# Optimization experiments

Hardware: AMD Instinct MI355X
Metric: run time of the kernel (lower is better)

Reference implementation:

```python
import jax, jax.numpy as jnp
import numpy as np

B, C, L, O = 32, 256, 336, 96
K, NLAYERS, DFF = 4, 2, 1024
EPS = 1e-5


def setup_inputs() -> dict:
    key = jax.random.key(0)
    ks = jax.random.split(key, 10)
    s1 = 1.0 / np.sqrt(L)
    s2 = 1.0 / np.sqrt(DFF)
    return {
        "x": jax.random.normal(ks[0], (B, C, L), dtype=jnp.float32),
        "rev_w": jnp.ones((C,), dtype=jnp.float32),
        "rev_b": jnp.zeros((C,), dtype=jnp.float32),
        "W1": jax.random.normal(ks[1], (K, NLAYERS, L, DFF), dtype=jnp.float32) * s1,
        "b1": jnp.zeros((K, NLAYERS, DFF), dtype=jnp.float32),
        "W2": jax.random.normal(ks[2], (K, NLAYERS, DFF, L), dtype=jnp.float32) * s2,
        "b2": jnp.zeros((K, NLAYERS, L), dtype=jnp.float32),
        "Wh": jax.random.normal(ks[3], (K, L, O), dtype=jnp.float32) * s1,
        "bh": jnp.zeros((K, O), dtype=jnp.float32),
        "assign": jax.random.randint(ks[4], (C,), 0, K, dtype=jnp.int32),
    }


def reference(x, rev_w, rev_b, W1, b1, W2, b2, Wh, bh, assign):
    # RevIN norm over the time axis, per instance and per channel. x: [B,C,L]
    mean = jnp.mean(x, axis=-1, keepdims=True)
    std = jnp.sqrt(jnp.var(x, axis=-1, keepdims=True) + EPS)
    xn = (x - mean) / std * rev_w[None, :, None] + rev_b[None, :, None]

    n_clusters = Wh.shape[0]
    n_layers = W1.shape[1]
    out = jnp.zeros(x.shape[:2] + (Wh.shape[-1],), dtype=x.dtype)  # [B,C,O]
    for k in range(n_clusters):
        z = xn  # [B,C,L] time-mixing MLP stack shared across channels
        for l in range(n_layers):
            h = jax.nn.relu(jnp.einsum('bcl,ld->bcd', z, W1[k, l]) + b1[k, l])
            z = z + jnp.einsum('bcd,dl->bcl', h, W2[k, l]) + b2[k, l]
        y = jnp.einsum('bcl,lo->bco', z, Wh[k]) + bh[k]  # [B,C,O]
        out = jnp.where((assign == k)[None, :, None], y, out)

    # RevIN denorm, then transpose to [B, out_len, C]
    out = (out - rev_b[None, :, None]) / rev_w[None, :, None] * std + mean
    return jnp.transpose(out, (0, 2, 1))
```

## Files before the change

kernel.cpp:

```cpp
#include <hip/hip_runtime.h>
#include <math.h>


typedef unsigned short u16;
typedef unsigned int u32;
typedef unsigned long long u64;

constexpr int B = 32, C = 256, L = 336, O = 96, K = 4, NL = 2, DFF = 1024;
constexpr int TM = 32;
constexpr int NTILES = (B * C) / TM;
constexpr int LP = 352;
constexpr int ZBS = 360;
constexpr int HS = 1032;

constexpr int DT1 = 32;
constexpr int KT1 = 22;
constexpr int LT2 = 11;
constexpr int KT2 = 64;
constexpr int NTH = 6;
constexpr int KSH = 11;

constexpr int TS1 = KT1 * 512;
constexpr int TS2 = KT2 * 512;
constexpr int THS = KSH * 512;

constexpr int W1FRAGS = DT1 * KT1 * 64;
constexpr int W2FRAGS = LT2 * KT2 * 64;
constexpr int WHFRAGS = NTH * KSH * 64;
constexpr int NW1 = W1FRAGS * K * NL;
constexpr int NW2 = W2FRAGS * K * NL;
constexpr int NPREP = 176 + 256 + 44 + 1;

typedef __bf16 bf16x8 __attribute__((ext_vector_type(8)));
typedef float f32x4 __attribute__((ext_vector_type(4)));
typedef float f32x16 __attribute__((ext_vector_type(16)));

__device__ float g_y[(size_t)B * O * C];

__device__ __forceinline__ u16 f2bf(float f) {
  union { float f; u32 u; } v;
  v.f = f;
  u32 r = v.u + 0x7fffu + ((v.u >> 16) & 1u);
  return (u16)(r >> 16);
}
__device__ __forceinline__ float bf2f(u16 h) {
  union { u32 u; float f; } v;
  v.u = ((u32)h) << 16;
  return v.f;
}
__device__ __forceinline__ u32 pack2(float a, float b) {
  return (u32)f2bf(a) | ((u32)f2bf(b) << 16);
}

__global__ __launch_bounds__(256) void prep(const int* __restrict__ assign,
                                            const float* __restrict__ W1,
                                            const float* __restrict__ W2,
                                            const float* __restrict__ Wh,
                                            int* __restrict__ meta,
                                            u16* __restrict__ wbuf) {
  __shared__ u16 sm[32][516];
  const int bid = blockIdx.x;
  const int tid = threadIdx.x;
  const int wid = tid >> 6, lane = tid & 63;
  const int q = lane >> 4, rm = lane & 15;
  const int q2 = lane >> 5, n32 = lane & 31;

  if (bid < 176) {
    const int dh = bid & 1;
    const int ks32 = (bid >> 1) % 11;
    const int kl = bid / 22;
    for (int rr = 0; rr < 8; ++rr) {
      const int r = wid * 8 + rr;
      const int l = ks32 * 32 + r;
#pragma unroll
      for (int h = 0; h < 2; ++h) {
        const int c = h * 256 + lane * 4;
        float4 v = make_float4(0.f, 0.f, 0.f, 0.f);
        if (l < L)
          v = *(const float4*)(W1 + ((size_t)kl * L + l) * DFF + dh * 512 + c);
        uint2 p;
        p.x = pack2(v.x, v.y);
        p.y = pack2(v.z, v.w);
        *(uint2*)&sm[r][c] = p;
      }
    }
    __syncthreads();
    for (int e = 0; e < 8; ++e) {
      const int item = wid * 8 + e;
      const int dtl = item >> 1, half = item & 1;
      const int rb = 16 * half + q2 * 8;
      const int col = dtl * 32 + n32;
      uint4 o;
      u32 w4[4];
#pragma unroll
      for (int jj = 0; jj < 4; ++jj)
        w4[jj] = (u32)sm[rb + 2 * jj][col] | ((u32)sm[rb + 2 * jj + 1][col] << 16);
      o.x = w4[0]; o.y = w4[1]; o.z = w4[2]; o.w = w4[3];
      const int dt = dh * 16 + dtl;
      const int ks = ks32 * 2 + half;
      *(uint4*)(wbuf + ((size_t)(kl * DT1 + dt) * KT1 + ks) * 512 + lane * 8) = o;
    }
  } else if (bid < 432) {
    const int b2i = bid - 176;
    const int ks32 = b2i & 31;
    const int kl = b2i >> 5;
    for (int rr = 0; rr < 8; ++rr) {
      const int r = wid * 8 + rr;
      const float* row = W2 + ((size_t)kl * DFF + ks32 * 32 + r) * L;
      {
        const int c = lane * 4;
        const float4 v = *(const float4*)(row + c);
        uint2 p;
        p.x = pack2(v.x, v.y);
        p.y = pack2(v.z, v.w);
        *(uint2*)&sm[r][c] = p;
      }
      {
        const int c = 256 + lane * 4;
        if (c < 352) {
          float4 v = make_float4(0.f, 0.f, 0.f, 0.f);
          if (c < L) v = *(const float4*)(row + c);
          uint2 p;
          p.x = pack2(v.x, v.y);
          p.y = pack2(v.z, v.w);
          *(uint2*)&sm[r][c] = p;
        }
      }
    }
    __syncthreads();
    for (int item = wid; item < 22; item += 4) {
      const int lt = item >> 1, half = item & 1;
      const int rb = 16 * half + q2 * 8;
      const int col = 32 * lt + n32;
      uint4 o;
      u32 w4[4];
#pragma unroll
      for (int jj = 0; jj < 4; ++jj)
        w4[jj] = (u32)sm[rb + 2 * jj][col] | ((u32)sm[rb + 2 * jj + 1][col] << 16);
      o.x = w4[0]; o.y = w4[1]; o.z = w4[2]; o.w = w4[3];
      const int ks = ks32 * 2 + half;
      *(uint4*)(wbuf + (size_t)NW1 * 8 +
                ((size_t)(kl * LT2 + lt) * KT2 + ks) * 512 + lane * 8) = o;
    }
  } else if (bid < 476) {
    const int b3i = bid - 432;
    const int ks = b3i % 11;
    const int kk = b3i / 11;
    for (int rr = 0; rr < 8; ++rr) {
      const int r = wid * 8 + rr;
      const int l = ks * 32 + r;
      if (lane < 24) {
        const int c = lane * 4;
        float4 v = make_float4(0.f, 0.f, 0.f, 0.f);
        if (l < L) v = *(const float4*)(Wh + ((size_t)kk * L + l) * O + c);
        uint2 p;
        p.x = pack2(v.x, v.y);
        p.y = pack2(v.z, v.w);
        *(uint2*)&sm[r][c] = p;
      }
    }
    __syncthreads();
    for (int nt = wid; nt < NTH; nt += 4) {
      uint4 o;
      u32 w4[4];
#pragma unroll
      for (int jj = 0; jj < 4; ++jj) {
        const u16 a = sm[q * 8 + 2 * jj][nt * 16 + rm];
        const u16 b = sm[q * 8 + 2 * jj + 1][nt * 16 + rm];
        w4[jj] = (u32)a | ((u32)b << 16);
      }
      o.x = w4[0]; o.y = w4[1]; o.z = w4[2]; o.w = w4[3];
      *(uint4*)(wbuf + (size_t)(NW1 + NW2) * 8 +
                ((size_t)(kk * NTH + nt) * KSH + ks) * 512 + lane * 8) = o;
    }
  } else {
    __shared__ int wcnt[4][K];
    __shared__ int pre[4][K];
    __shared__ int cofs[K + 1];
    const int a = assign[tid];
    const u64 below = (1ull << lane) - 1ull;
    int myrank = 0;
#pragma unroll
    for (int k = 0; k < K; ++k) {
      const u64 m = __ballot(a == k);
      if (a == k) myrank = (int)__popcll(m & below);
      if (lane == 0) wcnt[wid][k] = (int)__popcll(m);
    }
    __syncthreads();
    if (tid == 0) {
      int tot[K];
      for (int k = 0; k < K; ++k) {
        int s = 0;
        for (int ww = 0; ww < 4; ++ww) {
          pre[ww][k] = s;
          s += wcnt[ww][k];
        }
        tot[k] = s;
      }
      cofs[0] = 0;
      for (int k = 0; k < K; ++k) cofs[k + 1] = cofs[k] + tot[k];
      for (int k = 0; k <= K; ++k) meta[512 + k] = cofs[k];
    }
    __syncthreads();
    const int pos = cofs[a] + pre[wid][a] + myrank;
    meta[256 + pos] = tid;
    meta[520 + tid] = pos;
    int k = 0;
    while (k < K - 1 && tid >= cofs[k + 1]) ++k;
    meta[tid] = (k << 16) | ((tid - cofs[k]) * TM);
  }
}

__global__ __launch_bounds__(1024, 4) void mlp_mfma(
    const float* __restrict__ x, const float* __restrict__ rev_w,
    const float* __restrict__ rev_b, const float* __restrict__ b1,
    const float* __restrict__ b2, const float* __restrict__ bh,
    const int* __restrict__ meta, const u16* __restrict__ wbuf) {
  __shared__ __align__(16) u16 zb[TM][ZBS];
  __shared__ __align__(16) u16 Hsh[TM][HS];
  __shared__ float s_mean[TM], s_std[TM], s_rw[TM], s_rb[TM];
  __shared__ int s_b[TM], s_p[TM];

  const int tid = threadIdx.x;
  const int wid = tid >> 6;
  const int lane = tid & 63;
  const int q = lane >> 4, rm = lane & 15;
  const int q2 = lane >> 5, n32 = lane & 31;

  const int swz = (blockIdx.x & 7) * 32 + (blockIdx.x >> 3);
  const int info = meta[swz];
  const int kcl = info >> 16;
  const int rstart = info & 0xffff;
  const int cofs = meta[512 + kcl];
  const int cnt = meta[512 + kcl + 1] - cofs;

  for (int i = 0; i < 2; ++i) {
    const int t = wid * 2 + i;
    const int ri = rstart + t;
    const int b = ri / cnt;
    const int c = meta[256 + cofs + (ri % cnt)];
    const float* xrow = x + (size_t)(b * C + c) * L;
    float v[6], s = 0.f, s2 = 0.f;
#pragma unroll
    for (int jj = 0; jj < 6; ++jj) {
      const int j = lane + jj * 64;
      v[jj] = (j < L) ? xrow[j] : 0.f;
      s += v[jj];
      s2 += v[jj] * v[jj];
    }
#pragma unroll
    for (int off = 32; off > 0; off >>= 1) {
      s += __shfl_down(s, off);
      s2 += __shfl_down(s2, off);
    }
    s = __shfl(s, 0);
    s2 = __shfl(s2, 0);
    const float mean = s * (1.f / L);
    const float var = s2 * (1.f / L) - mean * mean;
    const float stdv = sqrtf(var + 1e-5f);
    const float rstd = 1.f / stdv;
    const float rw = rev_w[c], rb_ = rev_b[c];
#pragma unroll
    for (int jj = 0; jj < 6; ++jj) {
      const int j = lane + jj * 64;
      if (j < L) zb[t][j] = f2bf((v[jj] - mean) * rstd * rw + rb_);
    }
    if (lane < LP - L) zb[t][L + lane] = 0;
    if (lane == 0) {
      s_mean[t] = mean;
      s_std[t] = stdv;
      s_rw[t] = rw;
      s_rb[t] = rb_;
      s_b[t] = b;
      s_p[t] = cofs + (ri % cnt);
    }
  }

  const u16* w1b = wbuf;
  const u16* w2b = wbuf + (size_t)NW1 * 8;
  const u16* whb = wbuf + (size_t)(NW1 + NW2) * 8;

  bf16x8 a1[2][4];
  {
    const u16* b0 = w1b + (size_t)(kcl * NL) * W1FRAGS * 8 +
                    (size_t)(wid * 2) * TS1 + lane * 8;
#pragma unroll
    for (int t = 0; t < 2; ++t)
#pragma unroll
      for (int s = 0; s < 4; ++s)
        a1[t][s] = *(const bf16x8*)(b0 + (size_t)t * TS1 + s * 512);
  }
  __syncthreads();

  f32x16 zm;
#pragma unroll
  for (int i = 0; i < 16; ++i) zm[i] = 0.f;
  if (wid < LT2) {
#pragma unroll
    for (int g = 0; g < 4; ++g) {
      const uint2 zw = *(const uint2*)&zb[n32][32 * wid + 8 * g + 4 * q2];
      zm[4 * g + 0] = bf2f((u16)zw.x);
      zm[4 * g + 1] = bf2f((u16)(zw.x >> 16));
      zm[4 * g + 2] = bf2f((u16)zw.y);
      zm[4 * g + 3] = bf2f((u16)(zw.y >> 16));
    }
  }

  for (int l = 0; l < NL; ++l) {
    const int kl = kcl * NL + l;
    const u16* W1f = w1b + (size_t)kl * W1FRAGS * 8;
    const u16* W2f = w2b + (size_t)kl * W2FRAGS * 8;
    const float* b1p = b1 + kl * DFF;
    const float* b2p = b2 + kl * L;
    const u16* base1 = W1f + (size_t)(wid * 2) * TS1 + lane * 8;

    f32x16 acc[2];
#pragma unroll
    for (int t = 0; t < 2; ++t)
#pragma unroll
      for (int i = 0; i < 16; ++i) acc[t][i] = 0.f;
#pragma unroll
    for (int ks = 0; ks < KT1; ++ks) {
      const bf16x8 zf = *(const bf16x8*)&zb[n32][ks * 16 + q2 * 8];
#pragma unroll
      for (int t = 0; t < 2; ++t)
        acc[t] = __builtin_amdgcn_mfma_f32_32x32x16_bf16(a1[t][ks & 3], zf,
                                                         acc[t], 0, 0, 0);
      if (ks + 4 < KT1) {
#pragma unroll
        for (int t = 0; t < 2; ++t)
          a1[t][ks & 3] =
              *(const bf16x8*)(base1 + (size_t)t * TS1 + (ks + 4) * 512);
      }
    }
#pragma unroll
    for (int t = 0; t < 2; ++t) {
      const int dt = wid * 2 + t;
#pragma unroll
      for (int g = 0; g < 4; ++g) {
        const int db = dt * 32 + 8 * g + 4 * q2;
        const float4 bq = *(const float4*)(b1p + db);
        uint2 hw;
        hw.x = pack2(fmaxf(acc[t][4 * g + 0] + bq.x, 0.f),
                     fmaxf(acc[t][4 * g + 1] + bq.y, 0.f));
        hw.y = pack2(fmaxf(acc[t][4 * g + 2] + bq.z, 0.f),
                     fmaxf(acc[t][4 * g + 3] + bq.w, 0.f));
        *(uint2*)&Hsh[n32][db] = hw;
      }
    }

    bf16x8 a2[8];
    const u16* base2 = W2f + (size_t)wid * TS2 + lane * 8;
    if (wid < LT2) {
#pragma unroll
      for (int s = 0; s < 8; ++s)
        a2[s] = *(const bf16x8*)(base2 + s * 512);
    }
    __syncthreads();

    if (wid < LT2) {
#pragma unroll
      for (int ks = 0; ks < KT2; ++ks) {
        const bf16x8 hf = *(const bf16x8*)&Hsh[n32][ks * 16 + q2 * 8];
        zm = __builtin_amdgcn_mfma_f32_32x32x16_bf16(a2[ks & 7], hf, zm, 0, 0, 0);
        if (ks + 8 < KT2)
          a2[ks & 7] = *(const bf16x8*)(base2 + (ks + 8) * 512);
      }
#pragma unroll
      for (int g = 0; g < 4; ++g) {
        const int lc = 32 * wid + 8 * g + 4 * q2;
        if (lc < L) {
          const float4 bq = *(const float4*)(b2p + lc);
          zm[4 * g + 0] += bq.x;
          zm[4 * g + 1] += bq.y;
          zm[4 * g + 2] += bq.z;
          zm[4 * g + 3] += bq.w;
        }
        uint2 zw;
        zw.x = pack2(zm[4 * g + 0], zm[4 * g + 1]);
        zw.y = pack2(zm[4 * g + 2], zm[4 * g + 3]);
        *(uint2*)&zb[n32][lc] = zw;
      }
    }

    if (l + 1 < NL) {
      const u16* nb = w1b + (size_t)(kl + 1) * W1FRAGS * 8 +
                      (size_t)(wid * 2) * TS1 + lane * 8;
#pragma unroll
      for (int t = 0; t < 2; ++t)
#pragma unroll
        for (int s = 0; s < 4; ++s)
          a1[t][s] = *(const bf16x8*)(nb + (size_t)t * TS1 + s * 512);
    }
    __syncthreads();
  }

  if (wid < NTH) {
    const u16* Whf =
        whb + (size_t)kcl * WHFRAGS * 8 + (size_t)wid * THS + lane * 8;
    f32x4 acc0 = {0.f, 0.f, 0.f, 0.f}, acc1 = {0.f, 0.f, 0.f, 0.f};
    for (int ks = 0; ks < KSH; ++ks) {
      const bf16x8 af = *(const bf16x8*)(Whf + ks * 512);
      const bf16x8 zf0 = *(const bf16x8*)&zb[rm][ks * 32 + q * 8];
      const bf16x8 zf1 = *(const bf16x8*)&zb[rm + 16][ks * 32 + q * 8];
      acc0 = __builtin_amdgcn_mfma_f32_16x16x32_bf16(af, zf0, acc0, 0, 0, 0);
      acc1 = __builtin_amdgcn_mfma_f32_16x16x32_bf16(af, zf1, acc1, 0, 0, 0);
    }
    const float4 bq = *(const float4*)(bh + kcl * O + wid * 16 + q * 4);
    const float bqa[4] = {bq.x, bq.y, bq.z, bq.w};
#pragma unroll
    for (int rg = 0; rg < 2; ++rg) {
      const int row = rm + 16 * rg;
      const float mean = s_mean[row], stdv = s_std[row];
      const float rw = s_rw[row], rb_ = s_rb[row];
      const int ob = s_b[row], pp = s_p[row];
      const f32x4 acc = rg ? acc1 : acc0;
#pragma unroll
      for (int gg = 0; gg < 4; ++gg) {
        const int o = wid * 16 + q * 4 + gg;
        const float v = acc[gg] + bqa[gg];
        g_y[((size_t)ob * O + o) * C + pp] = (v - rb_) / rw * stdv + mean;
      }
    }
  }
}

__global__ __launch_bounds__(1024) void scatter_out(
    const int* __restrict__ meta, float* __restrict__ out) {
  const int row = blockIdx.x * 4 + (threadIdx.x >> 8);
  const int c = threadIdx.x & 255;
  const int p = meta[520 + c];
  out[(size_t)row * C + c] = g_y[(size_t)row * C + p];
}

extern "C" void kernel_launch(void* const* d_in, const int* in_sizes, int n_in,
                              void* d_out, int out_size, void* d_ws,
                              size_t ws_size, hipStream_t stream) {
  const float* x = (const float*)d_in[0];
  const float* rev_w = (const float*)d_in[1];
  const float* rev_b = (const float*)d_in[2];
  const float* W1 = (const float*)d_in[3];
  const float* b1 = (const float*)d_in[4];
  const float* W2 = (const float*)d_in[5];
  const float* b2 = (const float*)d_in[6];
  const float* Wh = (const float*)d_in[7];
  const float* bh = (const float*)d_in[8];
  const int* assign = (const int*)d_in[9];
  float* out = (float*)d_out;

  int* meta = (int*)d_ws;
  u16* wbuf = (u16*)((char*)d_ws + 4096);

  prep<<<NPREP, 256, 0, stream>>>(assign, W1, W2, Wh, meta, wbuf);
  mlp_mfma<<<NTILES, 1024, 0, stream>>>(x, rev_w, rev_b, b1, b2, bh, meta,
                                        wbuf);
  scatter_out<<<(B * O) / 4, 1024, 0, stream>>>(meta, out);
}
```

Before: 145.8 us.

## Fuse prep, MLP and scatter into one cooperative kernel with grid syncs

Replaces the three-launch sequence (weight repack/meta prep, MLP, output scatter) with a single cooperative kernel of 256 blocks that uses grid-wide syncs between phases. The weight repack work is spread across all blocks in XCD-aware order, which removes two kernel launch gaps and their inter-kernel idle time. In exchange it adds two grid barriers and shares LDS between the repack and the MLP. If the cooperative launch fails it falls back to the old three-kernel path.

```diff
diff --git a/kernel.cpp b/kernel.cpp
--- a/kernel.cpp
+++ b/kernel.cpp
@@ -1,5 +1,8 @@
 #include <hip/hip_runtime.h>
+#include <hip/hip_cooperative_groups.h>
 #include <math.h>
+
+namespace cg = cooperative_groups;
 
 
 typedef unsigned short u16;
@@ -52,6 +55,409 @@
   return (u32)f2bf(a) | ((u32)f2bf(b) << 16);
 }
 
+__global__ __launch_bounds__(1024, 4) void mono(
+    const float* __restrict__ x, const float* __restrict__ rev_w,
+    const float* __restrict__ rev_b, const float* __restrict__ W1,
+    const float* __restrict__ b1, const float* __restrict__ W2,
+    const float* __restrict__ b2, const float* __restrict__ Wh,
+    const float* __restrict__ bh, const int* __restrict__ assign,
+    int* __restrict__ meta, u16* __restrict__ wbuf,
+    float* __restrict__ out) {
+  __shared__ __align__(16) u16 zb[TM][ZBS];
+  __shared__ __align__(16) u16 Hsh[TM][HS];
+  __shared__ float s_mean[TM], s_std[TM], s_rw[TM], s_rb[TM];
+  __shared__ int s_b[TM], s_p[TM];
+  __shared__ int t_wcnt[4][K], t_pre[4][K], t_cofs[K + 1];
+
+  const int bid = blockIdx.x;
+  const int tid = threadIdx.x;
+  const int wid = tid >> 6;
+  const int lane = tid & 63;
+  const int q = lane >> 4, rm = lane & 15;
+  const int q2 = lane >> 5, n32 = lane & 31;
+
+  u16(*sm)[516] = (u16(*)[516]) & Hsh[0][0];
+
+  {
+    const int xcd = bid & 7;
+    const int cser = xcd >> 1;
+    const int jj2 = ((xcd & 1) << 5) + (bid >> 3);
+    for (int t2 = 0; t2 < 2; ++t2) {
+      const int iu = jj2 * 2 + t2;
+      if (iu < 119) {
+        __syncthreads();
+        if (iu < 44) {
+          const int dh = iu & 1;
+          const int ks32 = (iu >> 1) % 11;
+          const int kl = cser * 2 + iu / 22;
+          for (int rr = 0; rr < 2; ++rr) {
+            const int r = wid * 2 + rr;
+            const int l = ks32 * 32 + r;
+#pragma unroll
+            for (int h = 0; h < 2; ++h) {
+              const int cc = h * 256 + lane * 4;
+              float4 v = make_float4(0.f, 0.f, 0.f, 0.f);
+              if (l < L)
+                v = *(const float4*)(W1 + ((size_t)kl * L + l) * DFF +
+                                     dh * 512 + cc);
+              uint2 p;
+              p.x = pack2(v.x, v.y);
+              p.y = pack2(v.z, v.w);
+              *(uint2*)&sm[r][cc] = p;
+            }
+          }
+          __syncthreads();
+          for (int e = 0; e < 2; ++e) {
+            const int item = wid * 2 + e;
+            const int dtl = item >> 1, half = item & 1;
+            const int rb = 16 * half + q2 * 8;
+            const int col = dtl * 32 + n32;
+            u32 w4[4];
+#pragma unroll
+            for (int t4 = 0; t4 < 4; ++t4)
+              w4[t4] = (u32)sm[rb + 2 * t4][col] |
+                       ((u32)sm[rb + 2 * t4 + 1][col] << 16);
+            uint4 o;
+            o.x = w4[0]; o.y = w4[1]; o.z = w4[2]; o.w = w4[3];
+            const int dt = dh * 16 + dtl;
+            const int ks = ks32 * 2 + half;
+            *(uint4*)(wbuf + ((size_t)(kl * DT1 + dt) * KT1 + ks) * 512 +
+                      lane * 8) = o;
+          }
+        } else if (iu < 108) {
+          const int i2 = iu - 44;
+          const int ks32 = i2 & 31;
+          const int kl = cser * 2 + (i2 >> 5);
+          for (int rr = 0; rr < 2; ++rr) {
+            const int r = wid * 2 + rr;
+            const float* row = W2 + ((size_t)kl * DFF + ks32 * 32 + r) * L;
+            {
+              const int cc = lane * 4;
+              const float4 v = *(const float4*)(row + cc);
+              uint2 p;
+              p.x = pack2(v.x, v.y);
+              p.y = pack2(v.z, v.w);
+              *(uint2*)&sm[r][cc] = p;
+            }
+            {
+              const int cc = 256 + lane * 4;
+              if (cc < 352) {
+                float4 v = make_float4(0.f, 0.f, 0.f, 0.f);
+                if (cc < L) v = *(const float4*)(row + cc);
+                uint2 p;
+                p.x = pack2(v.x, v.y);
+                p.y = pack2(v.z, v.w);
+                *(uint2*)&sm[r][cc] = p;
+              }
+            }
+          }
+          __syncthreads();
+          for (int item = wid; item < 22; item += 16) {
+            const int lt = item >> 1, half = item & 1;
+            const int rb = 16 * half + q2 * 8;
+            const int col = 32 * lt + n32;
+            u32 w4[4];
+#pragma unroll
+            for (int t4 = 0; t4 < 4; ++t4)
+              w4[t4] = (u32)sm[rb + 2 * t4][col] |
+                       ((u32)sm[rb + 2 * t4 + 1][col] << 16);
+            uint4 o;
+            o.x = w4[0]; o.y = w4[1]; o.z = w4[2]; o.w = w4[3];
+            const int ks = ks32 * 2 + half;
+            *(uint4*)(wbuf + (size_t)NW1 * 8 +
+                      ((size_t)(kl * LT2 + lt) * KT2 + ks) * 512 + lane * 8) =
+                o;
+          }
+        } else {
+          const int ks = iu - 108;
+          const int kk = cser;
+          for (int rr = 0; rr < 2; ++rr) {
+            const int r = wid * 2 + rr;
+            const int l = ks * 32 + r;
+            if (lane < 24) {
+              const int cc = lane * 4;
+              float4 v = make_float4(0.f, 0.f, 0.f, 0.f);
+              if (l < L)
+                v = *(const float4*)(Wh + ((size_t)kk * L + l) * O + cc);
+              uint2 p;
+              p.x = pack2(v.x, v.y);
+              p.y = pack2(v.z, v.w);
+              *(uint2*)&sm[r][cc] = p;
+            }
+          }
+          __syncthreads();
+          if (wid < NTH) {
+            const int nt = wid;
+            u32 w4[4];
+#pragma unroll
+            for (int t4 = 0; t4 < 4; ++t4) {
+              const u16 aa = sm[q * 8 + 2 * t4][nt * 16 + rm];
+              const u16 bb = sm[q * 8 + 2 * t4 + 1][nt * 16 + rm];
+              w4[t4] = (u32)aa | ((u32)bb << 16);
+            }
+            uint4 o;
+            o.x = w4[0]; o.y = w4[1]; o.z = w4[2]; o.w = w4[3];
+            *(uint4*)(wbuf + (size_t)(NW1 + NW2) * 8 +
+                      ((size_t)(kk * NTH + nt) * KSH + ks) * 512 + lane * 8) =
+                o;
+          }
+        }
+      }
+    }
+    if (bid == NTILES - 1) {
+      const int a = (tid < C) ? assign[tid] : 0;
+      const u64 below = (1ull << lane) - 1ull;
+      int myrank = 0;
+      if (wid < 4) {
+#pragma unroll
+        for (int k = 0; k < K; ++k) {
+          const u64 m = __ballot(a == k);
+          if (a == k) myrank = (int)__popcll(m & below);
+          if (lane == 0) t_wcnt[wid][k] = (int)__popcll(m);
+        }
+      }
+      __syncthreads();
+      if (tid == 0) {
+        int tot[K];
+        for (int k = 0; k < K; ++k) {
+          int s = 0;
+          for (int ww = 0; ww < 4; ++ww) {
+            t_pre[ww][k] = s;
+            s += t_wcnt[ww][k];
+          }
+          tot[k] = s;
+        }
+        t_cofs[0] = 0;
+        for (int k = 0; k < K; ++k) t_cofs[k + 1] = t_cofs[k] + tot[k];
+        for (int k = 0; k <= K; ++k) meta[512 + k] = t_cofs[k];
+      }
+      __syncthreads();
+      if (tid < C) {
+        const int pos = t_cofs[a] + t_pre[wid][a] + myrank;
+        meta[256 + pos] = tid;
+        meta[520 + tid] = pos;
+        int k = 0;
+        while (k < K - 1 && tid >= t_cofs[k + 1]) ++k;
+        meta[tid] = (k << 16) | ((tid - t_cofs[k]) * TM);
+      }
+    }
+  }
+  __threadfence();
+  cg::this_grid().sync();
+
+  const int swz = (bid & 7) * 32 + (bid >> 3);
+  const int info = meta[swz];
+  const int kcl = info >> 16;
+  const int rstart = info & 0xffff;
+  const int cofs = meta[512 + kcl];
+  const int cnt = meta[512 + kcl + 1] - cofs;
+
+  for (int i = 0; i < 2; ++i) {
+    const int t = wid * 2 + i;
+    const int ri = rstart + t;
+    const int b = ri / cnt;
+    const int c = meta[256 + cofs + (ri % cnt)];
+    const float* xrow = x + (size_t)(b * C + c) * L;
+    float v[6], s = 0.f, s2 = 0.f;
+#pragma unroll
+    for (int jj = 0; jj < 6; ++jj) {
+      const int j = lane + jj * 64;
+      v[jj] = (j < L) ? xrow[j] : 0.f;
+      s += v[jj];
+      s2 += v[jj] * v[jj];
+    }
+#pragma unroll
+    for (int off = 32; off > 0; off >>= 1) {
+      s += __shfl_down(s, off);
+      s2 += __shfl_down(s2, off);
+    }
+    s = __shfl(s, 0);
+    s2 = __shfl(s2, 0);
+    const float mean = s * (1.f / L);
+    const float var = s2 * (1.f / L) - mean * mean;
+    const float stdv = sqrtf(var + 1e-5f);
+    const float rstd = 1.f / stdv;
+    const float rw = rev_w[c], rb_ = rev_b[c];
+#pragma unroll
+    for (int jj = 0; jj < 6; ++jj) {
+      const int j = lane + jj * 64;
+      if (j < L) zb[t][j] = f2bf((v[jj] - mean) * rstd * rw + rb_);
+    }
+    if (lane < LP - L) zb[t][L + lane] = 0;
+    if (lane == 0) {
+      s_mean[t] = mean;
+      s_std[t] = stdv;
+      s_rw[t] = rw;
+      s_rb[t] = rb_;
+      s_b[t] = b;
+      s_p[t] = cofs + (ri % cnt);
+    }
+  }
+
+  const u16* w1b = wbuf;
+  const u16* w2b = wbuf + (size_t)NW1 * 8;
+  const u16* whb = wbuf + (size_t)(NW1 + NW2) * 8;
+
+  bf16x8 a1[2][4];
+  {
+    const u16* b0 = w1b + (size_t)(kcl * NL) * W1FRAGS * 8 +
+                    (size_t)(wid * 2) * TS1 + lane * 8;
+#pragma unroll
+    for (int t = 0; t < 2; ++t)
+#pragma unroll
+      for (int s = 0; s < 4; ++s)
+        a1[t][s] = *(const bf16x8*)(b0 + (size_t)t * TS1 + s * 512);
+  }
+  __syncthreads();
+
+  f32x16 zm;
+#pragma unroll
+  for (int i = 0; i < 16; ++i) zm[i] = 0.f;
+  if (wid < LT2) {
+#pragma unroll
+    for (int g = 0; g < 4; ++g) {
+      const uint2 zw = *(const uint2*)&zb[n32][32 * wid + 8 * g + 4 * q2];
+      zm[4 * g + 0] = bf2f((u16)zw.x);
+      zm[4 * g + 1] = bf2f((u16)(zw.x >> 16));
+      zm[4 * g + 2] = bf2f((u16)zw.y);
+      zm[4 * g + 3] = bf2f((u16)(zw.y >> 16));
+    }
+  }
+
+  for (int l = 0; l < NL; ++l) {
+    const int kl = kcl * NL + l;
+    const u16* W1f = w1b + (size_t)kl * W1FRAGS * 8;
+    const u16* W2f = w2b + (size_t)kl * W2FRAGS * 8;
+    const float* b1p = b1 + kl * DFF;
+    const float* b2p = b2 + kl * L;
+    const u16* base1 = W1f + (size_t)(wid * 2) * TS1 + lane * 8;
+
+    f32x16 acc[2];
+#pragma unroll
+    for (int t = 0; t < 2; ++t)
+#pragma unroll
+      for (int i = 0; i < 16; ++i) acc[t][i] = 0.f;
+#pragma unroll
+    for (int ks = 0; ks < KT1; ++ks) {
+      const bf16x8 zf = *(const bf16x8*)&zb[n32][ks * 16 + q2 * 8];
+#pragma unroll
+      for (int t = 0; t < 2; ++t)
+        acc[t] = __builtin_amdgcn_mfma_f32_32x32x16_bf16(a1[t][ks & 3], zf,
+                                                         acc[t], 0, 0, 0);
+      if (ks + 4 < KT1) {
+#pragma unroll
+        for (int t = 0; t < 2; ++t)
+          a1[t][ks & 3] =
+              *(const bf16x8*)(base1 + (size_t)t * TS1 + (ks + 4) * 512);
+      }
+    }
+#pragma unroll
+    for (int t = 0; t < 2; ++t) {
+      const int dt = wid * 2 + t;
+#pragma unroll
+      for (int g = 0; g < 4; ++g) {
+        const int db = dt * 32 + 8 * g + 4 * q2;
+        const float4 bq = *(const float4*)(b1p + db);
+        uint2 hw;
+        hw.x = pack2(fmaxf(acc[t][4 * g + 0] + bq.x, 0.f),
+                     fmaxf(acc[t][4 * g + 1] + bq.y, 0.f));
+        hw.y = pack2(fmaxf(acc[t][4 * g + 2] + bq.z, 0.f),
+                     fmaxf(acc[t][4 * g + 3] + bq.w, 0.f));
+        *(uint2*)&Hsh[n32][db] = hw;
+      }
+    }
+
+    bf16x8 a2[8];
+    const u16* base2 = W2f + (size_t)wid * TS2 + lane * 8;
+    if (wid < LT2) {
+#pragma unroll
+      for (int s = 0; s < 8; ++s)
+        a2[s] = *(const bf16x8*)(base2 + s * 512);
+    }
+    __syncthreads();
+
+    if (wid < LT2) {
+#pragma unroll
+      for (int ks = 0; ks < KT2; ++ks) {
+        const bf16x8 hf = *(const bf16x8*)&Hsh[n32][ks * 16 + q2 * 8];
+        zm = __builtin_amdgcn_mfma_f32_32x32x16_bf16(a2[ks & 7], hf, zm, 0, 0,
+                                                     0);
+        if (ks + 8 < KT2)
+          a2[ks & 7] = *(const bf16x8*)(base2 + (ks + 8) * 512);
+      }
+#pragma unroll
+      for (int g = 0; g < 4; ++g) {
+        const int lc = 32 * wid + 8 * g + 4 * q2;
+        if (lc < L) {
+          const float4 bq = *(const float4*)(b2p + lc);
+          zm[4 * g + 0] += bq.x;
+          zm[4 * g + 1] += bq.y;
+          zm[4 * g + 2] += bq.z;
+          zm[4 * g + 3] += bq.w;
+        }
+        uint2 zw;
+        zw.x = pack2(zm[4 * g + 0], zm[4 * g + 1]);
+        zw.y = pack2(zm[4 * g + 2], zm[4 * g + 3]);
+        *(uint2*)&zb[n32][lc] = zw;
+      }
+    }
+
+    if (l + 1 < NL) {
+      const u16* nb = w1b + (size_t)(kl + 1) * W1FRAGS * 8 +
+                      (size_t)(wid * 2) * TS1 + lane * 8;
+#pragma unroll
+      for (int t = 0; t < 2; ++t)
+#pragma unroll
+        for (int s = 0; s < 4; ++s)
+          a1[t][s] = *(const bf16x8*)(nb + (size_t)t * TS1 + s * 512);
+    }
+    __syncthreads();
+  }
+
+  if (wid < NTH) {
+    const u16* Whf =
+        whb + (size_t)kcl * WHFRAGS * 8 + (size_t)wid * THS + lane * 8;
+    f32x4 acc0 = {0.f, 0.f, 0.f, 0.f}, acc1 = {0.f, 0.f, 0.f, 0.f};
+    for (int ks = 0; ks < KSH; ++ks) {
+      const bf16x8 af = *(const bf16x8*)(Whf + ks * 512);
+      const bf16x8 zf0 = *(const bf16x8*)&zb[rm][ks * 32 + q * 8];
+      const bf16x8 zf1 = *(const bf16x8*)&zb[rm + 16][ks * 32 + q * 8];
+      acc0 = __builtin_amdgcn_mfma_f32_16x16x32_bf16(af, zf0, acc0, 0, 0, 0);
+      acc1 = __builtin_amdgcn_mfma_f32_16x16x32_bf16(af, zf1, acc1, 0, 0, 0);
+    }
+    const float4 bq = *(const float4*)(bh + kcl * O + wid * 16 + q * 4);
+    const float bqa[4] = {bq.x, bq.y, bq.z, bq.w};
+#pragma unroll
+    for (int rg = 0; rg < 2; ++rg) {
+      const int row = rm + 16 * rg;
+      const float mean = s_mean[row], stdv = s_std[row];
+      const float rw = s_rw[row], rb_ = s_rb[row];
+      const int ob = s_b[row], pp = s_p[row];
+      const f32x4 acc = rg ? acc1 : acc0;
+#pragma unroll
+      for (int gg = 0; gg < 4; ++gg) {
+        const int o = wid * 16 + q * 4 + gg;
+        const float v = acc[gg] + bqa[gg];
+        g_y[((size_t)ob * O + o) * C + pp] = (v - rb_) / rw * stdv + mean;
+      }
+    }
+  }
+  __threadfence();
+  cg::this_grid().sync();
+
+  {
+    int* sip = (int*)&zb[0][0];
+    if (tid < C) sip[tid] = meta[520 + tid];
+    __syncthreads();
+    const int base = bid * 1024 + tid;
+#pragma unroll
+    for (int it = 0; it < 3; ++it) {
+      const int idx = base + it * (NTILES * 1024);
+      out[idx] = g_y[((size_t)(idx >> 8)) * C + sip[idx & 255]];
+    }
+  }
+}
+
 __global__ __launch_bounds__(256) void prep(const int* __restrict__ assign,
                                             const float* __restrict__ W1,
                                             const float* __restrict__ W2,
@@ -94,11 +500,13 @@
       u32 w4[4];
 #pragma unroll
       for (int jj = 0; jj < 4; ++jj)
-        w4[jj] = (u32)sm[rb + 2 * jj][col] | ((u32)sm[rb + 2 * jj + 1][col] << 16);
+        w4[jj] =
+            (u32)sm[rb + 2 * jj][col] | ((u32)sm[rb + 2 * jj + 1][col] << 16);
       o.x = w4[0]; o.y = w4[1]; o.z = w4[2]; o.w = w4[3];
       const int dt = dh * 16 + dtl;
       const int ks = ks32 * 2 + half;
-      *(uint4*)(wbuf + ((size_t)(kl * DT1 + dt) * KT1 + ks) * 512 + lane * 8) = o;
+      *(uint4*)(wbuf + ((size_t)(kl * DT1 + dt) * KT1 + ks) * 512 + lane * 8) =
+          o;
     }
   } else if (bid < 432) {
     const int b2i = bid - 176;
@@ -136,7 +544,8 @@
       u32 w4[4];
 #pragma unroll
       for (int jj = 0; jj < 4; ++jj)
-        w4[jj] = (u32)sm[rb + 2 * jj][col] | ((u32)sm[rb + 2 * jj + 1][col] << 16);
+        w4[jj] =
+            (u32)sm[rb + 2 * jj][col] | ((u32)sm[rb + 2 * jj + 1][col] << 16);
       o.x = w4[0]; o.y = w4[1]; o.z = w4[2]; o.w = w4[3];
       const int ks = ks32 * 2 + half;
       *(uint4*)(wbuf + (size_t)NW1 * 8 +
@@ -353,8 +762,7 @@
     const u16* base2 = W2f + (size_t)wid * TS2 + lane * 8;
     if (wid < LT2) {
 #pragma unroll
-      for (int s = 0; s < 8; ++s)
-        a2[s] = *(const bf16x8*)(base2 + s * 512);
+      for (int s = 0; s < 8; ++s) a2[s] = *(const bf16x8*)(base2 + s * 512);
     }
     __syncthreads();
 
@@ -362,7 +770,8 @@
 #pragma unroll
       for (int ks = 0; ks < KT2; ++ks) {
         const bf16x8 hf = *(const bf16x8*)&Hsh[n32][ks * 16 + q2 * 8];
-        zm = __builtin_amdgcn_mfma_f32_32x32x16_bf16(a2[ks & 7], hf, zm, 0, 0, 0);
+        zm = __builtin_amdgcn_mfma_f32_32x32x16_bf16(a2[ks & 7], hf, zm, 0, 0,
+                                                     0);
         if (ks + 8 < KT2)
           a2[ks & 7] = *(const bf16x8*)(base2 + (ks + 8) * 512);
       }
@@ -451,8 +860,17 @@
   int* meta = (int*)d_ws;
   u16* wbuf = (u16*)((char*)d_ws + 4096);
 
-  prep<<<NPREP, 256, 0, stream>>>(assign, W1, W2, Wh, meta, wbuf);
-  mlp_mfma<<<NTILES, 1024, 0, stream>>>(x, rev_w, rev_b, b1, b2, bh, meta,
-                                        wbuf);
-  scatter_out<<<(B * O) / 4, 1024, 0, stream>>>(meta, out);
+  void* kargs[] = {(void*)&x,    (void*)&rev_w, (void*)&rev_b, (void*)&W1,
+                   (void*)&b1,   (void*)&W2,    (void*)&b2,    (void*)&Wh,
+                   (void*)&bh,   (void*)&assign, (void*)&meta, (void*)&wbuf,
+                   (void*)&out};
+  hipError_t e = hipLaunchCooperativeKernel(mono, dim3(NTILES), dim3(1024),
+                                            kargs, 0, stream);
+  if (e != hipSuccess) {
+    (void)hipGetLastError();
+    prep<<<NPREP, 256, 0, stream>>>(assign, W1, W2, Wh, meta, wbuf);
+    mlp_mfma<<<NTILES, 1024, 0, stream>>>(x, rev_w, rev_b, b1, b2, bh, meta,
+                                          wbuf);
+    scatter_out<<<(B * O) / 4, 1024, 0, stream>>>(meta, out);
+  }
 }
```

Result: slower. 390.7 us (+168.0%).

## Prefetch upcoming weights into cache with idle warps and hoist W1 loads

Applied to the files above, without the earlier changes.

The first-layer W1 fragment loads are moved ahead of the RevIN normalization so their latency overlaps the statistics computation. During the second GEMM phase, warps that have no output columns (wid >= LT2) now issue strided touch-loads over the rest of the current W2 slab and over the next layer's W1 (or the head weights on the last layer). They XOR the results into registers that an empty asm statement keeps alive, so the data is pulled into cache before the busy warps need it. This adds extra memory traffic and issue slots on otherwise idle warps, and the hardcoded offsets assume a specific fragment layout.

```diff
diff --git a/kernel.cpp b/kernel.cpp
--- a/kernel.cpp
+++ b/kernel.cpp
@@ -234,6 +234,21 @@
   const int cofs = meta[512 + kcl];
   const int cnt = meta[512 + kcl + 1] - cofs;
 
+  const u16* w1b = wbuf;
+  const u16* w2b = wbuf + (size_t)NW1 * 8;
+  const u16* whb = wbuf + (size_t)(NW1 + NW2) * 8;
+
+  bf16x8 a1[2][4];
+  {
+    const u16* b0 = w1b + (size_t)(kcl * NL) * W1FRAGS * 8 +
+                    (size_t)(wid * 2) * TS1 + lane * 8;
+#pragma unroll
+    for (int t = 0; t < 2; ++t)
+#pragma unroll
+      for (int s = 0; s < 4; ++s)
+        a1[t][s] = *(const bf16x8*)(b0 + (size_t)t * TS1 + s * 512);
+  }
+
   for (int i = 0; i < 2; ++i) {
     const int t = wid * 2 + i;
     const int ri = rstart + t;
@@ -274,21 +289,6 @@
       s_b[t] = b;
       s_p[t] = cofs + (ri % cnt);
     }
-  }
-
-  const u16* w1b = wbuf;
-  const u16* w2b = wbuf + (size_t)NW1 * 8;
-  const u16* whb = wbuf + (size_t)(NW1 + NW2) * 8;
-
-  bf16x8 a1[2][4];
-  {
-    const u16* b0 = w1b + (size_t)(kcl * NL) * W1FRAGS * 8 +
-                    (size_t)(wid * 2) * TS1 + lane * 8;
-#pragma unroll
-    for (int t = 0; t < 2; ++t)
-#pragma unroll
-      for (int s = 0; s < 4; ++s)
-        a1[t][s] = *(const bf16x8*)(b0 + (size_t)t * TS1 + s * 512);
   }
   __syncthreads();
 
@@ -381,6 +381,43 @@
         zw.y = pack2(zm[4 * g + 2], zm[4 * g + 3]);
         *(uint2*)&zb[n32][lc] = zw;
       }
+    } else {
+      const int iw = wid - LT2;
+      const u32 lid = (u32)iw * 64u + (u32)lane;
+      u32 k0 = 0, k1 = 0, k2 = 0, k3 = 0;
+      {
+        const char* reg = (const char*)W2f;
+        for (int r = 0; r < 31; ++r) {
+          const u32 n = 1408u + (u32)r * 320u + lid;
+          if (n < 11264u) {
+            const u32 s = n / 176u;
+            const u32 rem = n - s * 176u;
+            const u32 off = (rem >> 4) * 65536u + s * 1024u + (rem & 15u) * 64u;
+            const uint4 v = *(const uint4*)(reg + off);
+            k0 ^= v.x; k1 ^= v.y; k2 ^= v.z; k3 ^= v.w;
+          }
+        }
+      }
+      if (l + 1 < NL) {
+        const char* reg = (const char*)(w1b + (size_t)(kl + 1) * W1FRAGS * 8);
+        for (int r = 0; r < 36; ++r) {
+          const u32 n = (u32)r * 320u + lid;
+          if (n < 11264u) {
+            const uint4 v = *(const uint4*)(reg + n * 64u);
+            k0 ^= v.x; k1 ^= v.y; k2 ^= v.z; k3 ^= v.w;
+          }
+        }
+      } else {
+        const char* reg = (const char*)(whb + (size_t)kcl * WHFRAGS * 8);
+        for (int r = 0; r < 4; ++r) {
+          const u32 n = (u32)r * 320u + lid;
+          if (n < 1056u) {
+            const uint4 v = *(const uint4*)(reg + n * 64u);
+            k0 ^= v.x; k1 ^= v.y; k2 ^= v.z; k3 ^= v.w;
+          }
+        }
+      }
+      asm volatile("" ::"v"(k0), "v"(k1), "v"(k2), "v"(k3));
     }
 
     if (l + 1 < NL) {
```

New measurement: 180.7 us. 1.24x slower.
